# Kernel optimization log

Hardware: AMD Instinct MI355X
Metric: run time of the kernel (lower is better)

The kernel has to match this reference:

```python
import jax, jax.numpy as jnp
import numpy as np

N = 100_000
E = 3_200_000
NCLASS = 64
TOPK = 16
NHID = 128
DEGREE = 6


def setup_inputs() -> dict:
    key = jax.random.key(0)
    ks = jax.random.split(key, 8)
    x = jax.random.normal(ks[0], (N, NCLASS), dtype=jnp.float32)
    edge_row = jax.random.randint(ks[1], (E,), 0, N, dtype=jnp.int64)
    edge_col = jax.random.randint(ks[2], (E,), 0, N, dtype=jnp.int64)
    edge_val = jax.random.uniform(ks[3], (E,), dtype=jnp.float32) / 32.0  # ~row-normalized
    # torch.nn.Linear init: U(-1/sqrt(fan_in), 1/sqrt(fan_in))
    lim1 = 1.0 / np.sqrt(TOPK)
    lim2 = 1.0 / np.sqrt(NHID)
    W1 = jax.random.uniform(ks[4], (NHID, TOPK), jnp.float32, -lim1, lim1)
    b1 = jnp.zeros((NHID,), jnp.float32)
    W2 = jax.random.uniform(ks[5], (DEGREE, NHID), jnp.float32, -lim2, lim2)
    b2 = jnp.zeros((DEGREE,), jnp.float32)
    return {"x": x, "edge_row": edge_row, "edge_col": edge_col,
            "edge_val": edge_val, "W1": W1, "b1": b1, "W2": W2, "b2": b2}


def _spmm(edge_row, edge_col, edge_val, h):
    # (adj @ h)[i] = sum_{(i,j) in E} val_ij * h[j]
    return jax.ops.segment_sum(edge_val[:, None] * h[edge_col], edge_row,
                               num_segments=N)


def reference(x, edge_row, edge_col, edge_val, W1, b1, W2, b2):
    # gating: softmax over classes -> top-k probs -> small MLP -> hop weights
    p = jax.nn.softmax(x, axis=1)
    tk, _ = jax.lax.top_k(p, TOPK)                       # [N, TOPK]
    h = jax.nn.leaky_relu(tk @ W1.T + b1, 0.1)           # [N, NHID]
    weight = jax.nn.softmax(h @ W2.T + b2, axis=1)       # [N, DEGREE]
    # dropout is identity in eval mode
    out = weight[:, 0:1] * x
    cur = x
    for i in range(DEGREE - 1):
        cur = _spmm(edge_row, edge_col, edge_val, cur)
        out = out + weight[:, i + 1:i + 2] * cur
    return jax.nn.log_softmax(out, axis=1)
```

## Files before the change

kernel.cpp:

```cpp
#include <hip/hip_runtime.h>
#include <math.h>

#define N_NODES 100000
#define N_EDGES 3200000
#define NCLASS  64
#define TOPK    16
#define NHID    128
#define DEG     6

#define NBUCK   391
#define NSEG    8
#define SEGCAP  1408

#define EB ((N_EDGES + 255) / 256)
#define GNODES 32
#define GB ((N_NODES + GNODES - 1) / GNODES)

__device__ __forceinline__ float bf2f(unsigned short u) {
    return __uint_as_float(((unsigned)u) << 16);
}
__device__ __forceinline__ unsigned short f2bf(float f) {
    unsigned u = __float_as_uint(f);
    u = (u + 0x7FFFu + ((u >> 16) & 1u)) >> 16;
    return (unsigned short)u;
}

__device__ __forceinline__ float wave_max(float v) {
    #pragma unroll
    for (int off = 1; off < 64; off <<= 1) v = fmaxf(v, __shfl_xor(v, off));
    return v;
}
__device__ __forceinline__ float wave_sum(float v) {
    #pragma unroll
    for (int off = 1; off < 64; off <<= 1) v += __shfl_xor(v, off);
    return v;
}

__global__ __launch_bounds__(256) void scatter_gating_kernel(
        const int* __restrict__ erow, const int* __restrict__ ecol,
        const float* __restrict__ eval, int* __restrict__ fill,
        int2* __restrict__ staging,
        const float* __restrict__ x,  const float* __restrict__ W1,
        const float* __restrict__ b1, const float* __restrict__ W2,
        const float* __restrict__ b2, float* __restrict__ weight,
        float* __restrict__ out_acc, unsigned short* __restrict__ xbf) {
    __shared__ float sW1t[TOPK * NHID];
    __shared__ float sb1[NHID];
    __shared__ float sW2[DEG * NHID];
    __shared__ float sb2[DEG];

    unsigned bi = blockIdx.x;
    if (bi % 5 != 0) {
        int sid = (int)(bi - bi / 5u - 1u);
        int i = sid * 256 + threadIdx.x;
        int s = (int)(bi & 7u);
        if (i < N_EDGES) {
            int   r = __builtin_nontemporal_load(&erow[i]);
            int   c = __builtin_nontemporal_load(&ecol[i]);
            float w = __builtin_nontemporal_load(&eval[i]);
            int b = r >> 8;
            int pos = atomicAdd(&fill[(s * NBUCK + b) * 16], 1);
            if (pos < SEGCAP) {
                int2 e;
                e.x = (c << 8) | (r & 255);
                e.y = __float_as_int(w);
                staging[((size_t)b * NSEG + s) * SEGCAP + pos] = e;
            }
        }
        return;
    }

    int gb = (int)(bi / 5u);
    int tid = threadIdx.x;
    for (int idx = tid; idx < NHID * TOPK; idx += 256) {
        int k = idx / NHID, j = idx - k * NHID;
        sW1t[idx] = W1[j * TOPK + k];
    }
    for (int i = tid; i < NHID; i += 256) sb1[i] = b1[i];
    for (int i = tid; i < DEG * NHID; i += 256) sW2[i] = W2[i];
    if (tid < DEG) sb2[tid] = b2[tid];
    __syncthreads();

    int wave = tid >> 6;
    int lane = tid & 63;

    for (int it = 0; it < GNODES / 4; it++) {
        int node = gb * GNODES + it * 4 + wave;
        if (node >= N_NODES) continue;

        float xv = x[node * NCLASS + lane];
        xbf[node * NCLASS + lane] = f2bf(xv);

        float v = xv;
        #pragma unroll
        for (int k = 2; k <= 64; k <<= 1) {
            #pragma unroll
            for (int j = k >> 1; j > 0; j >>= 1) {
                float o = __shfl_xor(v, j);
                bool keep_small = (((lane & j) == 0) == ((lane & k) == 0));
                v = keep_small ? fminf(v, o) : fmaxf(v, o);
            }
        }
        float m = __shfl(v, 63);
        float e = __expf(v - m);
        float s = wave_sum(e);
        float inv_s = 1.0f / s;

        float h0 = sb1[lane], h1 = sb1[lane + 64];
        #pragma unroll
        for (int k = 0; k < TOPK; k++) {
            float sv = __shfl(v, 63 - k);
            float tk = __expf(sv - m) * inv_s;
            h0 += tk * sW1t[k * NHID + lane];
            h1 += tk * sW1t[k * NHID + lane + 64];
        }
        h0 = (h0 > 0.f) ? h0 : 0.1f * h0;
        h1 = (h1 > 0.f) ? h1 : 0.1f * h1;

        float w[DEG];
        float wm = -1e30f;
        #pragma unroll
        for (int d = 0; d < DEG; d++) {
            float part = h0 * sW2[d * NHID + lane] + h1 * sW2[d * NHID + lane + 64];
            w[d] = wave_sum(part) + sb2[d];
            wm = fmaxf(wm, w[d]);
        }
        float wsum = 0.f;
        #pragma unroll
        for (int d = 0; d < DEG; d++) { w[d] = __expf(w[d] - wm); wsum += w[d]; }
        float inv = 1.0f / wsum;

        if (lane < DEG) weight[node * DEG + lane] = w[lane] * inv;
        out_acc[node * NCLASS + lane] = w[0] * inv * xv;
    }
}

__global__ __launch_bounds__(256) void phase2_build(
        const int2* __restrict__ staging, const int* __restrict__ fill,
        int* __restrict__ row_ptr, int2* __restrict__ edges_s) {
    __shared__ int lred[256];
    __shared__ int lhist[256];
    __shared__ int lscan[256];
    __shared__ int lfill[256];
    __shared__ int sseg[NSEG];
    int b = blockIdx.x, tid = threadIdx.x;

    int part = 0;
    for (int j = tid; j < b; j += 256) {
        int t = 0;
        #pragma unroll
        for (int s = 0; s < NSEG; s++) t += min(fill[(s * NBUCK + j) * 16], SEGCAP);
        part += t;
    }
    lred[tid] = part;
    if (tid < NSEG) sseg[tid] = min(fill[(tid * NBUCK + b) * 16], SEGCAP);
    __syncthreads();
    for (int off = 128; off > 0; off >>= 1) {
        if (tid < off) lred[tid] += lred[tid + off];
        __syncthreads();
    }
    int base_b = lred[0];

    lhist[tid] = 0;
    __syncthreads();
    for (int s = 0; s < NSEG; s++) {
        int c = sseg[s];
        const int2* seg = staging + ((size_t)b * NSEG + s) * SEGCAP;
        for (int j = tid; j < c; j += 256) atomicAdd(&lhist[seg[j].x & 255], 1);
    }
    __syncthreads();
    int v = lhist[tid];
    lscan[tid] = v;
    __syncthreads();
    for (int off = 1; off < 256; off <<= 1) {
        int t = (tid >= off) ? lscan[tid - off] : 0;
        __syncthreads();
        lscan[tid] += t;
        __syncthreads();
    }
    int excl = base_b + (lscan[tid] - v);
    int grow = b * 256 + tid;
    if (grow < N_NODES) row_ptr[grow] = excl;
    if (b == NBUCK - 1 && tid == 255) row_ptr[N_NODES] = excl + v;
    lfill[tid] = excl;
    __syncthreads();
    for (int s = 0; s < NSEG; s++) {
        int c = sseg[s];
        const int2* seg = staging + ((size_t)b * NSEG + s) * SEGCAP;
        for (int j = tid; j < c; j += 256) {
            int2 e = seg[j];
            int rl = e.x & 255;
            int pos = atomicAdd(&lfill[rl], 1);
            edges_s[pos] = make_int2((int)(((unsigned)e.x) >> 8), e.y);
        }
    }
}

__device__ __forceinline__ void gather8(const unsigned short* __restrict__ src,
                                        const long long* __restrict__ edq,
                                        int e, int lane, float& acc) {
    long long q[8];
    #pragma unroll
    for (int k = 0; k < 8; k++) q[k] = __builtin_nontemporal_load(&edq[e + k]);
    float vk[8], fk[8];
    #pragma unroll
    for (int k = 0; k < 8; k++) {
        int col = __builtin_amdgcn_readfirstlane((int)(unsigned)q[k]);
        vk[k] = __int_as_float(__builtin_amdgcn_readfirstlane((int)(q[k] >> 32)));
        fk[k] = bf2f(src[col * NCLASS + lane]);
    }
    #pragma unroll
    for (int k = 0; k < 8; k++) acc += vk[k] * fk[k];
}

__device__ __forceinline__ void gather4(const unsigned short* __restrict__ src,
                                        const long long* __restrict__ edq,
                                        int e, int lane, float& acc) {
    long long q[4];
    #pragma unroll
    for (int k = 0; k < 4; k++) q[k] = __builtin_nontemporal_load(&edq[e + k]);
    float vk[4], fk[4];
    #pragma unroll
    for (int k = 0; k < 4; k++) {
        int col = __builtin_amdgcn_readfirstlane((int)(unsigned)q[k]);
        vk[k] = __int_as_float(__builtin_amdgcn_readfirstlane((int)(q[k] >> 32)));
        fk[k] = bf2f(src[col * NCLASS + lane]);
    }
    #pragma unroll
    for (int k = 0; k < 4; k++) acc += vk[k] * fk[k];
}

__device__ __forceinline__ float drain_row(const unsigned short* __restrict__ src,
                                           const long long* __restrict__ edq,
                                           int e, int end, int lane, float acc) {
    for (; e + 4 <= end; e += 4) gather4(src, edq, e, lane, acc);
    for (; e < end; e++) {
        long long q0 = __builtin_nontemporal_load(&edq[e]);
        int   c0 = __builtin_amdgcn_readfirstlane((int)(unsigned)q0);
        float v0 = __int_as_float(__builtin_amdgcn_readfirstlane((int)(q0 >> 32)));
        acc += v0 * bf2f(src[c0 * NCLASS + lane]);
    }
    return acc;
}

__global__ __launch_bounds__(256) void spmm_kernel(
        const unsigned short* __restrict__ src, unsigned short* __restrict__ dst,
        const unsigned short* __restrict__ prev2,
        const int* __restrict__ row_ptr, const int2* __restrict__ edges_s,
        const float* __restrict__ weight,
        float* __restrict__ out_acc, float* __restrict__ final_out,
        int hop, int mode) {
    int wave = threadIdx.x >> 6;
    int lane = threadIdx.x & 63;
    int wid = blockIdx.x * 4 + wave;
    int r0 = wid * 4;
    if (r0 >= N_NODES) return;

    int p0 = __builtin_amdgcn_readfirstlane(row_ptr[r0]);
    int p1 = __builtin_amdgcn_readfirstlane(row_ptr[r0 + 1]);
    int p2 = __builtin_amdgcn_readfirstlane(row_ptr[r0 + 2]);
    int p3 = __builtin_amdgcn_readfirstlane(row_ptr[r0 + 3]);
    int p4 = __builtin_amdgcn_readfirstlane(row_ptr[r0 + 4]);

    const long long* edq = (const long long*)edges_s;
    float acc[4] = {0.f, 0.f, 0.f, 0.f};
    int e0 = p0, e1 = p1, e2 = p2, e3 = p3;
    while (e0 + 8 <= p1 && e1 + 8 <= p2 && e2 + 8 <= p3 && e3 + 8 <= p4) {
        gather8(src, edq, e0, lane, acc[0]);
        gather8(src, edq, e1, lane, acc[1]);
        gather8(src, edq, e2, lane, acc[2]);
        gather8(src, edq, e3, lane, acc[3]);
        e0 += 8; e1 += 8; e2 += 8; e3 += 8;
    }
    acc[0] = drain_row(src, edq, e0, p1, lane, acc[0]);
    acc[1] = drain_row(src, edq, e1, p2, lane, acc[1]);
    acc[2] = drain_row(src, edq, e2, p3, lane, acc[2]);
    acc[3] = drain_row(src, edq, e3, p4, lane, acc[3]);

    #pragma unroll
    for (int k = 0; k < 4; k++) {
        int r = r0 + k;
        float a = acc[k];
        float w = weight[r * DEG + hop];
        if (mode == 0) {
            dst[r * NCLASS + lane] = f2bf(a);
        } else if (mode == 1) {
            dst[r * NCLASS + lane] = f2bf(a);
            float p  = bf2f(src[r * NCLASS + lane]);
            float wp = weight[r * DEG + hop - 1];
            out_acc[r * NCLASS + lane] += wp * p + w * a;
        } else {
            float q1 = bf2f(src[r * NCLASS + lane]);
            float q2 = bf2f(prev2[r * NCLASS + lane]);
            float v = out_acc[r * NCLASS + lane]
                    + weight[r * DEG + hop - 2] * q2
                    + weight[r * DEG + hop - 1] * q1 + w * a;
            float m = wave_max(v);
            float ee = __expf(v - m);
            float ss = wave_sum(ee);
            final_out[r * NCLASS + lane] = v - m - __logf(ss);
        }
    }
}

extern "C" void kernel_launch(void* const* d_in, const int* in_sizes, int n_in,
                              void* d_out, int out_size, void* d_ws, size_t ws_size,
                              hipStream_t stream) {
    const float* x    = (const float*)d_in[0];
    const int*   erow = (const int*)  d_in[1];
    const int*   ecol = (const int*)  d_in[2];
    const float* eval = (const float*)d_in[3];
    const float* W1   = (const float*)d_in[4];
    const float* b1   = (const float*)d_in[5];
    const float* W2   = (const float*)d_in[6];
    const float* b2   = (const float*)d_in[7];
    float* out = (float*)d_out;

    char* ws = (char*)d_ws;
    size_t off = 0;
    auto alloc = [&](size_t bytes) -> void* {
        void* p = ws + off;
        off = (off + bytes + 255) & ~(size_t)255;
        return p;
    };
    char* regionS = (char*)alloc((size_t)NBUCK * NSEG * SEGCAP * 8);
    int2* staging = (int2*)regionS;
    unsigned short* cur0 = (unsigned short*)regionS;
    unsigned short* cur1 = (unsigned short*)(regionS + (size_t)N_NODES * NCLASS * 2);
    unsigned short* xbf  = (unsigned short*)alloc((size_t)N_NODES * NCLASS * 2);

    int2*  edges_s = (int2*)alloc((size_t)N_EDGES * 8);
    int*   row_ptr = (int*) alloc((size_t)(N_NODES + 1) * 4);
    int*   fill    = (int*) alloc((size_t)NSEG * NBUCK * 16 * 4);
    float* weight  = (float*)alloc((size_t)N_NODES * DEG * 4);

    const int WB = (N_NODES / 4 + 3) / 4;

    hipMemsetAsync(fill, 0, (size_t)NSEG * NBUCK * 16 * 4, stream);
    scatter_gating_kernel<<<EB + GB, 256, 0, stream>>>(
        erow, ecol, eval, fill, staging, x, W1, b1, W2, b2, weight, out, xbf);
    phase2_build<<<NBUCK, 256, 0, stream>>>(staging, fill, row_ptr, edges_s);

    spmm_kernel<<<WB, 256, 0, stream>>>(xbf,  cur0, cur0, row_ptr, edges_s, weight, out, out, 1, 0);
    spmm_kernel<<<WB, 256, 0, stream>>>(cur0, cur1, cur0, row_ptr, edges_s, weight, out, out, 2, 1);
    spmm_kernel<<<WB, 256, 0, stream>>>(cur1, cur0, cur0, row_ptr, edges_s, weight, out, out, 3, 0);
    spmm_kernel<<<WB, 256, 0, stream>>>(cur0, cur1, cur0, row_ptr, edges_s, weight, out, out, 4, 0);
    spmm_kernel<<<WB, 256, 0, stream>>>(cur1, cur0, cur0, row_ptr, edges_s, weight, out, out, 5, 3);
}
```

Before: 667.1 us.

## Gather eight edges per wave with 16-byte bf16 row loads and lane-group reduction

Restructures the SpMM inner loop. Each wave now loads up to 64 edge records cooperatively, then splits into 8 lane groups of 8 lanes; each group fetches a whole neighbour row as uint4 (8 bf16 per lane), so 8 edges are gathered per step. Partial sums are reduced across the groups with shuffles, and the epilogue is vectorised over 8 lanes with packed stores. The cost being targeted is the per-lane 2-byte gathers and scalar readfirstlane edge decoding. In exchange it adds shuffle-reduction overhead, leaves 56 of 64 lanes idle in the epilogue, and pads the edge buffer so the wide edge loads stay in bounds.

```diff
diff --git a/kernel.cpp b/kernel.cpp
--- a/kernel.cpp
+++ b/kernel.cpp
@@ -23,6 +23,12 @@
     unsigned u = __float_as_uint(f);
     u = (u + 0x7FFFu + ((u >> 16) & 1u)) >> 16;
     return (unsigned short)u;
+}
+__device__ __forceinline__ void unpk8(uint4 d, float* f) {
+    f[0] = __uint_as_float(d.x << 16); f[1] = __uint_as_float(d.x & 0xffff0000u);
+    f[2] = __uint_as_float(d.y << 16); f[3] = __uint_as_float(d.y & 0xffff0000u);
+    f[4] = __uint_as_float(d.z << 16); f[5] = __uint_as_float(d.z & 0xffff0000u);
+    f[6] = __uint_as_float(d.w << 16); f[7] = __uint_as_float(d.w & 0xffff0000u);
 }
 
 __device__ __forceinline__ float wave_max(float v) {
@@ -196,53 +202,6 @@
     }
 }
 
-__device__ __forceinline__ void gather8(const unsigned short* __restrict__ src,
-                                        const long long* __restrict__ edq,
-                                        int e, int lane, float& acc) {
-    long long q[8];
-    #pragma unroll
-    for (int k = 0; k < 8; k++) q[k] = __builtin_nontemporal_load(&edq[e + k]);
-    float vk[8], fk[8];
-    #pragma unroll
-    for (int k = 0; k < 8; k++) {
-        int col = __builtin_amdgcn_readfirstlane((int)(unsigned)q[k]);
-        vk[k] = __int_as_float(__builtin_amdgcn_readfirstlane((int)(q[k] >> 32)));
-        fk[k] = bf2f(src[col * NCLASS + lane]);
-    }
-    #pragma unroll
-    for (int k = 0; k < 8; k++) acc += vk[k] * fk[k];
-}
-
-__device__ __forceinline__ void gather4(const unsigned short* __restrict__ src,
-                                        const long long* __restrict__ edq,
-                                        int e, int lane, float& acc) {
-    long long q[4];
-    #pragma unroll
-    for (int k = 0; k < 4; k++) q[k] = __builtin_nontemporal_load(&edq[e + k]);
-    float vk[4], fk[4];
-    #pragma unroll
-    for (int k = 0; k < 4; k++) {
-        int col = __builtin_amdgcn_readfirstlane((int)(unsigned)q[k]);
-        vk[k] = __int_as_float(__builtin_amdgcn_readfirstlane((int)(q[k] >> 32)));
-        fk[k] = bf2f(src[col * NCLASS + lane]);
-    }
-    #pragma unroll
-    for (int k = 0; k < 4; k++) acc += vk[k] * fk[k];
-}
-
-__device__ __forceinline__ float drain_row(const unsigned short* __restrict__ src,
-                                           const long long* __restrict__ edq,
-                                           int e, int end, int lane, float acc) {
-    for (; e + 4 <= end; e += 4) gather4(src, edq, e, lane, acc);
-    for (; e < end; e++) {
-        long long q0 = __builtin_nontemporal_load(&edq[e]);
-        int   c0 = __builtin_amdgcn_readfirstlane((int)(unsigned)q0);
-        float v0 = __int_as_float(__builtin_amdgcn_readfirstlane((int)(q0 >> 32)));
-        acc += v0 * bf2f(src[c0 * NCLASS + lane]);
-    }
-    return acc;
-}
-
 __global__ __launch_bounds__(256) void spmm_kernel(
         const unsigned short* __restrict__ src, unsigned short* __restrict__ dst,
         const unsigned short* __restrict__ prev2,
@@ -256,49 +215,127 @@
     int r0 = wid * 4;
     if (r0 >= N_NODES) return;
 
-    int p0 = __builtin_amdgcn_readfirstlane(row_ptr[r0]);
-    int p1 = __builtin_amdgcn_readfirstlane(row_ptr[r0 + 1]);
-    int p2 = __builtin_amdgcn_readfirstlane(row_ptr[r0 + 2]);
-    int p3 = __builtin_amdgcn_readfirstlane(row_ptr[r0 + 3]);
-    int p4 = __builtin_amdgcn_readfirstlane(row_ptr[r0 + 4]);
+    int p[5];
+    #pragma unroll
+    for (int k = 0; k < 5; k++)
+        p[k] = __builtin_amdgcn_readfirstlane(row_ptr[r0 + k]);
+
+    int g  = lane >> 3;
+    int co = (lane & 7) * 8;
 
     const long long* edq = (const long long*)edges_s;
-    float acc[4] = {0.f, 0.f, 0.f, 0.f};
-    int e0 = p0, e1 = p1, e2 = p2, e3 = p3;
-    while (e0 + 8 <= p1 && e1 + 8 <= p2 && e2 + 8 <= p3 && e3 + 8 <= p4) {
-        gather8(src, edq, e0, lane, acc[0]);
-        gather8(src, edq, e1, lane, acc[1]);
-        gather8(src, edq, e2, lane, acc[2]);
-        gather8(src, edq, e3, lane, acc[3]);
-        e0 += 8; e1 += 8; e2 += 8; e3 += 8;
-    }
-    acc[0] = drain_row(src, edq, e0, p1, lane, acc[0]);
-    acc[1] = drain_row(src, edq, e1, p2, lane, acc[1]);
-    acc[2] = drain_row(src, edq, e2, p3, lane, acc[2]);
-    acc[3] = drain_row(src, edq, e3, p4, lane, acc[3]);
+
+    float acc[4][8];
+    #pragma unroll
+    for (int k = 0; k < 4; k++)
+        #pragma unroll
+        for (int j = 0; j < 8; j++) acc[k][j] = 0.f;
 
     #pragma unroll
     for (int k = 0; k < 4; k++) {
-        int r = r0 + k;
-        float a = acc[k];
-        float w = weight[r * DEG + hop];
-        if (mode == 0) {
-            dst[r * NCLASS + lane] = f2bf(a);
-        } else if (mode == 1) {
-            dst[r * NCLASS + lane] = f2bf(a);
-            float p  = bf2f(src[r * NCLASS + lane]);
-            float wp = weight[r * DEG + hop - 1];
-            out_acc[r * NCLASS + lane] += wp * p + w * a;
-        } else {
-            float q1 = bf2f(src[r * NCLASS + lane]);
-            float q2 = bf2f(prev2[r * NCLASS + lane]);
-            float v = out_acc[r * NCLASS + lane]
-                    + weight[r * DEG + hop - 2] * q2
-                    + weight[r * DEG + hop - 1] * q1 + w * a;
-            float m = wave_max(v);
-            float ee = __expf(v - m);
-            float ss = wave_sum(ee);
-            final_out[r * NCLASS + lane] = v - m - __logf(ss);
+        int pr = p[k], nnz = p[k + 1] - pr;
+        for (int base = 0; base < nnz; base += 64) {
+            long long q = __builtin_nontemporal_load(&edq[pr + base + lane]);
+            int qc = (int)(unsigned)q;
+            float qw = __int_as_float((int)(q >> 32));
+            int rem = nnz - base;
+            int ng = ((rem < 64 ? rem : 64) + 7) >> 3;
+            for (int t = 0; t < ng; t++) {
+                int lsel = t * 8 + g;
+                int colb = __shfl(qc, lsel);
+                float wb = __shfl(qw, lsel);
+                wb = (t * 8 + g < rem) ? wb : 0.f;
+                uint4 d = *(const uint4*)(src + colb * NCLASS + co);
+                acc[k][0] += wb * __uint_as_float(d.x << 16);
+                acc[k][1] += wb * __uint_as_float(d.x & 0xffff0000u);
+                acc[k][2] += wb * __uint_as_float(d.y << 16);
+                acc[k][3] += wb * __uint_as_float(d.y & 0xffff0000u);
+                acc[k][4] += wb * __uint_as_float(d.z << 16);
+                acc[k][5] += wb * __uint_as_float(d.z & 0xffff0000u);
+                acc[k][6] += wb * __uint_as_float(d.w << 16);
+                acc[k][7] += wb * __uint_as_float(d.w & 0xffff0000u);
+            }
+        }
+        #pragma unroll
+        for (int j = 0; j < 8; j++) {
+            float v = acc[k][j];
+            v += __shfl_xor(v, 8);
+            v += __shfl_xor(v, 16);
+            v += __shfl_xor(v, 32);
+            acc[k][j] = v;
+        }
+    }
+
+    if (lane < 8) {
+        #pragma unroll
+        for (int k = 0; k < 4; k++) {
+            int r = r0 + k;
+            float w = weight[r * DEG + hop];
+            int boff = r * NCLASS + lane * 8;
+            float a_[8];
+            #pragma unroll
+            for (int j = 0; j < 8; j++) a_[j] = acc[k][j];
+
+            if (mode == 0 || mode == 1) {
+                uint4 st;
+                st.x = (unsigned)f2bf(a_[0]) | ((unsigned)f2bf(a_[1]) << 16);
+                st.y = (unsigned)f2bf(a_[2]) | ((unsigned)f2bf(a_[3]) << 16);
+                st.z = (unsigned)f2bf(a_[4]) | ((unsigned)f2bf(a_[5]) << 16);
+                st.w = (unsigned)f2bf(a_[6]) | ((unsigned)f2bf(a_[7]) << 16);
+                *(uint4*)(dst + boff) = st;
+                if (mode == 1) {
+                    float wp = weight[r * DEG + hop - 1];
+                    float pv[8];
+                    unpk8(*(const uint4*)(src + boff), pv);
+                    float4 o0 = *(float4*)(out_acc + boff);
+                    float4 o1 = *(float4*)(out_acc + boff + 4);
+                    o0.x += wp * pv[0] + w * a_[0];
+                    o0.y += wp * pv[1] + w * a_[1];
+                    o0.z += wp * pv[2] + w * a_[2];
+                    o0.w += wp * pv[3] + w * a_[3];
+                    o1.x += wp * pv[4] + w * a_[4];
+                    o1.y += wp * pv[5] + w * a_[5];
+                    o1.z += wp * pv[6] + w * a_[6];
+                    o1.w += wp * pv[7] + w * a_[7];
+                    *(float4*)(out_acc + boff)     = o0;
+                    *(float4*)(out_acc + boff + 4) = o1;
+                }
+            } else {
+                float w2v = weight[r * DEG + hop - 2];
+                float w1v = weight[r * DEG + hop - 1];
+                float q1v[8], q2v[8];
+                unpk8(*(const uint4*)(src + boff),   q1v);
+                unpk8(*(const uint4*)(prev2 + boff), q2v);
+                float4 o0 = *(float4*)(out_acc + boff);
+                float4 o1 = *(float4*)(out_acc + boff + 4);
+                float v[8];
+                v[0] = o0.x + w2v * q2v[0] + w1v * q1v[0] + w * a_[0];
+                v[1] = o0.y + w2v * q2v[1] + w1v * q1v[1] + w * a_[1];
+                v[2] = o0.z + w2v * q2v[2] + w1v * q1v[2] + w * a_[2];
+                v[3] = o0.w + w2v * q2v[3] + w1v * q1v[3] + w * a_[3];
+                v[4] = o1.x + w2v * q2v[4] + w1v * q1v[4] + w * a_[4];
+                v[5] = o1.y + w2v * q2v[5] + w1v * q1v[5] + w * a_[5];
+                v[6] = o1.z + w2v * q2v[6] + w1v * q1v[6] + w * a_[6];
+                v[7] = o1.w + w2v * q2v[7] + w1v * q1v[7] + w * a_[7];
+                float m = v[0];
+                #pragma unroll
+                for (int j = 1; j < 8; j++) m = fmaxf(m, v[j]);
+                m = fmaxf(m, __shfl_xor(m, 1));
+                m = fmaxf(m, __shfl_xor(m, 2));
+                m = fmaxf(m, __shfl_xor(m, 4));
+                float s = 0.f;
+                #pragma unroll
+                for (int j = 0; j < 8; j++) s += __expf(v[j] - m);
+                s += __shfl_xor(s, 1);
+                s += __shfl_xor(s, 2);
+                s += __shfl_xor(s, 4);
+                float ls = m + __logf(s);
+                float4 f0, f1;
+                f0.x = v[0] - ls; f0.y = v[1] - ls; f0.z = v[2] - ls; f0.w = v[3] - ls;
+                f1.x = v[4] - ls; f1.y = v[5] - ls; f1.z = v[6] - ls; f1.w = v[7] - ls;
+                *(float4*)(final_out + boff)     = f0;
+                *(float4*)(final_out + boff + 4) = f1;
+            }
         }
     }
 }
@@ -329,7 +366,7 @@
     unsigned short* cur1 = (unsigned short*)(regionS + (size_t)N_NODES * NCLASS * 2);
     unsigned short* xbf  = (unsigned short*)alloc((size_t)N_NODES * NCLASS * 2);
 
-    int2*  edges_s = (int2*)alloc((size_t)N_EDGES * 8);
+    int2*  edges_s = (int2*)alloc((size_t)N_EDGES * 8 + 512);
     int*   row_ptr = (int*) alloc((size_t)(N_NODES + 1) * 4);
     int*   fill    = (int*) alloc((size_t)NSEG * NBUCK * 16 * 4);
     float* weight  = (float*)alloc((size_t)N_NODES * DEG * 4);
@@ -337,6 +374,7 @@
     const int WB = (N_NODES / 4 + 3) / 4;
 
     hipMemsetAsync(fill, 0, (size_t)NSEG * NBUCK * 16 * 4, stream);
+    hipMemsetAsync(edges_s + N_EDGES, 0, 512, stream);
     scatter_gating_kernel<<<EB + GB, 256, 0, stream>>>(
         erow, ecol, eval, fill, staging, x, W1, b1, W2, b2, weight, out, xbf);
     phase2_build<<<NBUCK, 256, 0, stream>>>(staging, fill, row_ptr, edges_s);
```

Result: slower. 710.2 us (+6.5%).
